# Kernel tuning notes

Hardware: AMD Instinct MI355X
Metric: run time of the kernel (lower is better)

## Reference

```python
import jax, jax.numpy as jnp
import numpy as np

EMBED_DIM = 2048
NUM_HEADS = 32
NUM_SEQS = 8
SEQ_LEN = 1024
TOTAL_TOKENS = NUM_SEQS * SEQ_LEN


def setup_inputs() -> dict:
    key = jax.random.key(0)
    ks = jax.random.split(key, 9)
    E = EMBED_DIM
    std = 0.02
    return {
        "hidden_states": jax.random.normal(ks[0], (TOTAL_TOKENS, E), dtype=jnp.float32),
        "Wq": jax.random.normal(ks[1], (E, E), dtype=jnp.float32) * std,
        "bq": jax.random.normal(ks[2], (E,), dtype=jnp.float32) * std,
        "Wk": jax.random.normal(ks[3], (E, E), dtype=jnp.float32) * std,
        "bk": jax.random.normal(ks[4], (E,), dtype=jnp.float32) * std,
        "Wv": jax.random.normal(ks[5], (E, E), dtype=jnp.float32) * std,
        "bv": jax.random.normal(ks[6], (E,), dtype=jnp.float32) * std,
        "Wo": jax.random.normal(ks[7], (E, E), dtype=jnp.float32) * std,
        "bo": jax.random.normal(ks[8], (E,), dtype=jnp.float32) * std,
        "seq_len": SEQ_LEN,
    }


def reference(hidden_states, Wq, bq, Wk, bk, Wv, bv, Wo, bo, seq_len):
    # OPTAttention (has_cache=False): block-diagonal causal attention over
    # packed ragged sequences; here all NUM_SEQS sequences have length seq_len,
    # so the block-diagonal mask is exactly per-sequence causal attention.
    T, E = hidden_states.shape
    H = NUM_HEADS
    D = E // H
    B = T // seq_len
    scaling = D ** -0.5

    # torch nn.Linear: y = x @ W.T + b
    q = hidden_states @ Wq.T + bq
    k = hidden_states @ Wk.T + bk
    v = hidden_states @ Wv.T + bv

    q = q.reshape(B, seq_len, H, D)
    k = k.reshape(B, seq_len, H, D)
    v = v.reshape(B, seq_len, H, D)

    # [B, H, S, S] attention scores (xformers applies scale to q@k.T)
    scores = jnp.einsum("bqhd,bkhd->bhqk", q, k) * scaling
    causal = jnp.tril(jnp.ones((seq_len, seq_len), dtype=bool))
    scores = jnp.where(causal[None, None, :, :], scores, jnp.finfo(scores.dtype).min)
    probs = jax.nn.softmax(scores, axis=-1)

    attn = jnp.einsum("bhqk,bkhd->bqhd", probs, v)  # [B, S, H, D]
    attn = attn.reshape(T, E)
    return attn @ Wo.T + bo
```

## Files before the change

### kernel.cpp

```cpp
#include <hip/hip_runtime.h>
#include <hip/hip_bf16.h>

typedef __bf16 bf16_t;
typedef __bf16 bf16x8 __attribute__((ext_vector_type(8)));
typedef __bf16 bf16x4 __attribute__((ext_vector_type(4)));
typedef float f32x4 __attribute__((ext_vector_type(4)));
typedef float f32x16 __attribute__((ext_vector_type(16)));
typedef unsigned short u16x8 __attribute__((ext_vector_type(8)));
typedef unsigned int u32x4 __attribute__((ext_vector_type(4)));

#define T_TOK 8192
#define E_DIM 2048
#define NHEAD 32
#define SEQLEN 1024
#define NSEQ 8
#define LDQ 6144

#if __has_builtin(__builtin_amdgcn_exp2f)
#define EXP2F(x) __builtin_amdgcn_exp2f(x)
#else
#define EXP2F(x) exp2f(x)
#endif

static __device__ inline unsigned cvtpk_bf16(float lo, float hi) {
    unsigned r;
    asm("v_cvt_pk_bf16_f32 %0, %1, %2" : "=v"(r) : "v"(lo), "v"(hi));
    return r;
}

static __device__ inline void plswap(unsigned &x, unsigned &y, bool lo_half) {
#if __has_builtin(__builtin_amdgcn_permlane32_swap)
    auto r = __builtin_amdgcn_permlane32_swap(x, y, false, false);
    x = r[0]; y = r[1];
#else
    unsigned xs = __shfl_xor(x, 32), ys = __shfl_xor(y, 32);
    unsigned nx = lo_half ? x : ys;
    unsigned ny = lo_half ? xs : y;
    x = nx; y = ny;
#endif
}

__global__ void cvt_all(const float* __restrict__ hid, const float* __restrict__ Wq,
                        const float* __restrict__ Wk, const float* __restrict__ Wv,
                        const float* __restrict__ Wo, bf16_t* __restrict__ hidB,
                        bf16_t* __restrict__ Wcat, bf16_t* __restrict__ WoB) {
    const int TE4 = (T_TOK * E_DIM) / 4;
    const int EE4 = (E_DIM * E_DIM) / 4;
    const float* src;
    bf16_t* dst;
    int n4, base, nb;
    const int bid = blockIdx.x;
    if (bid < 2048)      { src = hid; dst = hidB;              n4 = TE4; base = 0;    nb = 2048; }
    else if (bid < 2560) { src = Wq;  dst = Wcat;              n4 = EE4; base = 2048; nb = 512; }
    else if (bid < 3072) { src = Wk;  dst = Wcat + 4 * EE4;    n4 = EE4; base = 2560; nb = 512; }
    else if (bid < 3584) { src = Wv;  dst = Wcat + 8 * EE4;    n4 = EE4; base = 3072; nb = 512; }
    else                 { src = Wo;  dst = WoB;               n4 = EE4; base = 3584; nb = 512; }
    const int stride = nb * 256;
    for (int i = (bid - base) * 256 + threadIdx.x; i < n4; i += stride) {
        const float4 v = reinterpret_cast<const float4*>(src)[i];
        bf16x4 o;
        o[0] = (bf16_t)v.x; o[1] = (bf16_t)v.y; o[2] = (bf16_t)v.z; o[3] = (bf16_t)v.w;
        reinterpret_cast<bf16x4*>(dst)[i] = o;
    }
}

template<bool OUT_BF16>
__global__ __launch_bounds__(512, 2)
void gemm256f(const bf16_t* __restrict__ A, const bf16_t* __restrict__ B,
              const float* __restrict__ b0, const float* __restrict__ b1,
              const float* __restrict__ b2, void* __restrict__ Cout,
              int M, int N, float qs, int qlim) {
    constexpr int K = 2048;
    constexpr int NK = K / 32;
    __shared__ alignas(16) unsigned char lds[131072];
    const int tid = threadIdx.x;
    const int wid = tid >> 6, l = tid & 63;
    const int cpx = gridDim.x >> 3;
    const int wg = (blockIdx.x & 7) * cpx + (blockIdx.x >> 3);
    const int nbm = M >> 8;
    const int bm = wg % nbm, bn = wg / nbm;
    const int wrow = (wid >> 2) * 128, wcol = (wid & 3) * 64;
    const int lr = l & 15, lg = l >> 4;

    f32x4 acc[8][4] = {};

    const bf16_t* aBase = A + (size_t)(bm * 256) * K;
    const bf16_t* bBase = B + (size_t)(bn * 256) * K;
    const int sr = l >> 2;
    const int sc = (l & 3) * 16;

    auto stage = [&](int t) {
        unsigned char* base = lds + (t & 3) * 32768;
#pragma unroll
        for (int c = 0; c < 2; ++c) {
            const int chunk = wid * 2 + c;
            const int r = chunk * 16 + sr;
            const int cb = sc ^ (((r >> 1) & 3) << 4);
            __builtin_amdgcn_global_load_lds(
                (const __attribute__((address_space(1))) void*)(aBase + (size_t)r * K + t * 32 + (cb >> 1)),
                (__attribute__((address_space(3))) void*)(base + chunk * 1024), 16, 0, 0);
            __builtin_amdgcn_global_load_lds(
                (const __attribute__((address_space(1))) void*)(bBase + (size_t)r * K + t * 32 + (cb >> 1)),
                (__attribute__((address_space(3))) void*)(base + 16384 + chunk * 1024), 16, 0, 0);
        }
    };

    bf16x8 fa0[8], fb0[4], fa1[8], fb1[4];

    stage(0); stage(1); stage(2);
    asm volatile("s_waitcnt vmcnt(4)" ::: "memory");
    __builtin_amdgcn_s_barrier();
    {
        const unsigned char* Ab = lds;
        const unsigned char* Bb = Ab + 16384;
#pragma unroll
        for (int n = 0; n < 4; ++n) {
            const int r = wcol + n * 16 + lr;
            fb0[n] = *reinterpret_cast<const bf16x8*>(Bb + r * 64 + ((lg * 16) ^ (((r >> 1) & 3) << 4)));
        }
#pragma unroll
        for (int m = 0; m < 8; ++m) {
            const int r = wrow + m * 16 + lr;
            fa0[m] = *reinterpret_cast<const bf16x8*>(Ab + r * 64 + ((lg * 16) ^ (((r >> 1) & 3) << 4)));
        }
    }

    auto step = [&](int t, bf16x8 (&ca)[8], bf16x8 (&cb)[4],
                    bf16x8 (&na)[8], bf16x8 (&nb)[4]) {
        if (t + 3 < NK) stage(t + 3);
        const unsigned char* Nb = lds + ((t + 1) & 3) * 32768;
        const unsigned char* NbB = Nb + 16384;
        __builtin_amdgcn_s_setprio(1);
#pragma unroll
        for (int m = 0; m < 8; ++m) {
            if (m < 4) {
                const int rb = wcol + m * 16 + lr;
                nb[m] = *reinterpret_cast<const bf16x8*>(NbB + rb * 64 + ((lg * 16) ^ (((rb >> 1) & 3) << 4)));
            }
            const int ra = wrow + m * 16 + lr;
            na[m] = *reinterpret_cast<const bf16x8*>(Nb + ra * 64 + ((lg * 16) ^ (((ra >> 1) & 3) << 4)));
#pragma unroll
            for (int n = 0; n < 4; ++n)
                acc[m][n] = __builtin_amdgcn_mfma_f32_16x16x32_bf16(ca[m], cb[n], acc[m][n], 0, 0, 0);
        }
        __builtin_amdgcn_s_setprio(0);
        if (t < NK - 1) {
            if (t + 3 < NK) asm volatile("s_waitcnt vmcnt(4)" ::: "memory");
            else            asm volatile("s_waitcnt vmcnt(0)" ::: "memory");
            __builtin_amdgcn_s_barrier();
        }
    };

#pragma unroll 1
    for (int t = 0; t < NK; t += 2) {
        step(t,     fa0, fb0, fa1, fb1);
        step(t + 1, fa1, fb1, fa0, fb0);
    }

    const int r0 = bm * 256 + wrow + lg * 4;
    const int c0 = bn * 256 + wcol + lr;
#pragma unroll
    for (int n = 0; n < 4; ++n) {
        const int cc = c0 + n * 16;
        const float bias = (cc < 2048) ? b0[cc] : (cc < 4096 ? b1[cc - 2048] : b2[cc - 4096]);
        const float sc2 = (cc < qlim) ? qs : 1.0f;
#pragma unroll
        for (int m = 0; m < 8; ++m)
#pragma unroll
            for (int j = 0; j < 4; ++j) {
                const int rr = r0 + m * 16 + j;
                const float v = (acc[m][n][j] + bias) * sc2;
                if (OUT_BF16) ((bf16_t*)Cout)[(size_t)rr * N + cc] = (bf16_t)v;
                else          ((float*)Cout)[(size_t)rr * N + cc] = v;
            }
    }
}

__global__ __launch_bounds__(512, 2)
void attn_fwd3(const bf16_t* __restrict__ QKV, bf16_t* __restrict__ Og) {
    const int orig = blockIdx.x;
    const int id = (orig & 7) * 64 + (orig >> 3);
    const int grp = id >> 1;
    const int pairIdx = id & 1;
    const int h = grp & 31;
    const int sq = grp >> 5;

    const int tid = threadIdx.x;
    const int w = tid >> 6;
    const int l = tid & 63;
    const int ll = l & 31;
    const int hi = l >> 5;
    const bool lo_half = (hi == 0);

    __shared__ alignas(16) unsigned char lds[65536];

    const bf16_t* Qg = QKV;
    const bf16_t* Kg = QKV + 2048;
    const bf16_t* Vg = QKV + 4096;
    const size_t kvbase = (size_t)(sq * SEQLEN) * LDQ + h * 64;

    bf16x8 vr0, vr1;
    const int vk0 = l * 2;
    const int vd0 = w * 8;

    auto stageK = [&](int kt, int buf) {
#pragma unroll
        for (int c = 0; c < 2; ++c) {
            const int o = (w * 2 + c) * 1024 + l * 16;
            const int r = o >> 7;
            const int swb = (o & 127) ^ ((r & 7) << 4);
            const bf16_t* src = Kg + kvbase + (size_t)(kt * 128 + r) * LDQ + (swb >> 1);
            __builtin_amdgcn_global_load_lds(
                (const __attribute__((address_space(1))) void*)src,
                (__attribute__((address_space(3))) void*)(lds + buf * 16384 + (w * 2 + c) * 1024),
                16, 0, 0);
        }
    };
    auto loadV = [&](int kt) {
        const bf16_t* vp = Vg + kvbase + (size_t)(kt * 128 + vk0) * LDQ + vd0;
        vr0 = *reinterpret_cast<const bf16x8*>(vp);
        vr1 = *reinterpret_cast<const bf16x8*>(vp + LDQ);
    };
    auto writeV = [&](int buf) {
        u16x8 s0 = __builtin_bit_cast(u16x8, vr0);
        u16x8 s1 = __builtin_bit_cast(u16x8, vr1);
        unsigned char* vb = lds + 32768 + buf * 16384;
#pragma unroll
        for (int e = 0; e < 8; ++e) {
            const int d = vd0 + e;
            unsigned off = (unsigned)(d * 256 + vk0 * 2);
            off ^= ((unsigned)((d ^ (d >> 4)) & 15)) << 4;
            *reinterpret_cast<unsigned*>(vb + off) = (unsigned)s0[e] | ((unsigned)s1[e] << 16);
        }
    };

    const unsigned ksw = (unsigned)((l & 7) << 4);
    const unsigned kbase = (unsigned)(ll * 128 + hi * 16);

#pragma unroll 1
    for (int seg = 0; seg < 2; ++seg) {
        const int qt = pairIdx ? (seg ? 2 : 1) : (seg ? 3 : 0);

        const int q_glob = qt * 256 + w * 32 + ll;
        const bf16_t* qp = Qg + (size_t)(sq * SEQLEN + q_glob) * LDQ + h * 64 + hi * 8;
        bf16x8 qf[4];
#pragma unroll
        for (int dc = 0; dc < 4; ++dc)
            qf[dc] = *reinterpret_cast<const bf16x8*>(qp + dc * 16);

        const int nkt = 2 * qt + 2;
        const int q_wave_max = qt * 256 + w * 32 + 31;

        f32x16 oac[2] = {};
        float mrun = -3.0e38f, lsum = 0.f;

        stageK(0, 0);
        loadV(0);
        writeV(0);
        __syncthreads();

        int cur = 0;
        for (int kt = 0; kt < nkt; ++kt) {
            const bool notlast = (kt + 1 < nkt);
            if (notlast) { stageK(kt + 1, cur ^ 1); loadV(kt + 1); }

            if (kt * 128 <= q_wave_max) {
                const unsigned char* Kcur = lds + cur * 16384;
                const unsigned char* Vcur = lds + 32768 + cur * 16384;

                f32x16 st[4];
#pragma unroll
                for (int kh = 0; kh < 4; ++kh) {
                    f32x16 acc = {};
#pragma unroll
                    for (int dc = 0; dc < 4; ++dc) {
                        const unsigned off = (kbase + (unsigned)(kh * 4096 + dc * 32)) ^ ksw;
                        const bf16x8 ka = *reinterpret_cast<const bf16x8*>(Kcur + off);
                        acc = __builtin_amdgcn_mfma_f32_32x32x16_bf16(ka, qf[dc], acc, 0, 0, 0);
                    }
                    st[kh] = acc;
                }

                if (kt >= 2 * qt) {
#pragma unroll
                    for (int kh = 0; kh < 4; ++kh)
#pragma unroll
                        for (int r = 0; r < 16; ++r) {
                            const int kg = kt * 128 + kh * 32 + (r & 3) + 8 * (r >> 2) + 4 * hi;
                            if (kg > q_glob) st[kh][r] = -3.0e38f;
                        }
                }

                float tm = -3.0e38f;
#pragma unroll
                for (int kh = 0; kh < 4; ++kh)
#pragma unroll
                    for (int r = 0; r < 16; ++r) tm = fmaxf(tm, st[kh][r]);
                tm = fmaxf(tm, __shfl_xor(tm, 32));

                if (!__all(tm <= mrun + 8.0f)) {
                    const float mnew = fmaxf(mrun, tm);
                    const float rsc = EXP2F(mrun - mnew);
                    mrun = mnew;
                    lsum *= rsc;
#pragma unroll
                    for (int dh = 0; dh < 2; ++dh)
#pragma unroll
                        for (int r = 0; r < 16; ++r) oac[dh][r] *= rsc;
                }

                float ps = 0.f;
#pragma unroll
                for (int kh = 0; kh < 4; ++kh)
#pragma unroll
                    for (int r = 0; r < 16; ++r) {
                        const float p = EXP2F(st[kh][r] - mrun);
                        st[kh][r] = p;
                        ps += p;
                    }
                ps += __shfl_xor(ps, 32);
                lsum += ps;

                bf16x8 pf[8];
#pragma unroll
                for (int kh = 0; kh < 4; ++kh)
#pragma unroll
                    for (int hc = 0; hc < 2; ++hc) {
                        const int b0i = hc * 8;
                        unsigned a  = cvtpk_bf16(st[kh][b0i + 0], st[kh][b0i + 1]);
                        unsigned b  = cvtpk_bf16(st[kh][b0i + 4], st[kh][b0i + 5]);
                        unsigned a2 = cvtpk_bf16(st[kh][b0i + 2], st[kh][b0i + 3]);
                        unsigned b2 = cvtpk_bf16(st[kh][b0i + 6], st[kh][b0i + 7]);
                        plswap(a, b, lo_half);
                        plswap(a2, b2, lo_half);
                        u32x4 words = { a, a2, b, b2 };
                        pf[kh * 2 + hc] = __builtin_bit_cast(bf16x8, words);
                    }

#pragma unroll
                for (int dh = 0; dh < 2; ++dh) {
                    const int d = dh * 32 + ll;
                    const unsigned vsw = ((unsigned)((d ^ (d >> 4)) & 15)) << 4;
                    const unsigned vbb = (unsigned)(d * 256 + hi * 16);
#pragma unroll
                    for (int kc = 0; kc < 8; ++kc) {
                        const unsigned off = (vbb + (unsigned)(kc * 32)) ^ vsw;
                        const bf16x8 vfr = *reinterpret_cast<const bf16x8*>(Vcur + off);
                        oac[dh] = __builtin_amdgcn_mfma_f32_32x32x16_bf16(vfr, pf[kc], oac[dh], 0, 0, 0);
                    }
                }
            }

            if (notlast) writeV(cur ^ 1);
            __syncthreads();
            cur ^= 1;
        }

        const float inv = 1.0f / lsum;
        bf16_t* op = Og + (size_t)(sq * SEQLEN + q_glob) * E_DIM + h * 64;
#pragma unroll
        for (int dh = 0; dh < 2; ++dh)
#pragma unroll
            for (int rq = 0; rq < 4; ++rq) {
                const int d0 = dh * 32 + 8 * rq + 4 * hi;
                bf16x4 ov;
#pragma unroll
                for (int j = 0; j < 4; ++j)
                    ov[j] = (bf16_t)(oac[dh][rq * 4 + j] * inv);
                *reinterpret_cast<bf16x4*>(op + d0) = ov;
            }
    }
}

extern "C" void kernel_launch(void* const* d_in, const int* in_sizes, int n_in,
                              void* d_out, int out_size, void* d_ws, size_t ws_size,
                              hipStream_t stream) {
    const float* hid = (const float*)d_in[0];
    const float* Wq  = (const float*)d_in[1];
    const float* bq  = (const float*)d_in[2];
    const float* Wk  = (const float*)d_in[3];
    const float* bk  = (const float*)d_in[4];
    const float* Wv  = (const float*)d_in[5];
    const float* bv  = (const float*)d_in[6];
    const float* Wo  = (const float*)d_in[7];
    const float* bo  = (const float*)d_in[8];
    float* out = (float*)d_out;

    const size_t TE = (size_t)T_TOK * E_DIM;
    const size_t EE = (size_t)E_DIM * E_DIM;

    bf16_t* ws   = (bf16_t*)d_ws;
    bf16_t* hidB = ws;
    bf16_t* qkvB = ws + TE;
    bf16_t* Wcat = qkvB + 3 * TE;
    bf16_t* WoB  = Wcat + 3 * EE;

    cvt_all<<<4096, 256, 0, stream>>>(hid, Wq, Wk, Wv, Wo, hidB, Wcat, WoB);

    const float QSCALE = 0.125f * 1.4426950408889634f;

    gemm256f<true><<<dim3((T_TOK / 256) * (LDQ / 256)), 512, 0, stream>>>(
        hidB, Wcat, bq, bk, bv, qkvB, T_TOK, LDQ, QSCALE, 2048);

    attn_fwd3<<<dim3(512), 512, 0, stream>>>(qkvB, hidB);

    gemm256f<false><<<dim3((T_TOK / 256) * (E_DIM / 256)), 512, 0, stream>>>(
        hidB, WoB, bo, bo, bo, out, T_TOK, E_DIM, 1.0f, 0);
}
```

Measured before the change: 397.9 us.

## Restructure GEMM into 8-phase pipeline with K=64 tiles and half-tile staging

Replaces the GEMM main loop with a schedule that uses 64-wide K tiles double-buffered in LDS. Each K step is split into four MFMA quadrants, and staging of the next tiles' A/B halves is interleaved between barrier-separated phases. The aim is to overlap global-to-LDS loads, LDS reads and MFMA more evenly and to halve the number of loop iterations. In exchange it adds many more barriers per iteration, which may stall waves, and it changes the LDS swizzle, which affects bank-conflict behaviour.

```diff
diff --git a/kernel.cpp b/kernel.cpp
--- a/kernel.cpp
+++ b/kernel.cpp
@@ -66,12 +66,12 @@
 
 template<bool OUT_BF16>
 __global__ __launch_bounds__(512, 2)
-void gemm256f(const bf16_t* __restrict__ A, const bf16_t* __restrict__ B,
-              const float* __restrict__ b0, const float* __restrict__ b1,
-              const float* __restrict__ b2, void* __restrict__ Cout,
-              int M, int N, float qs, int qlim) {
+void gemm8p(const bf16_t* __restrict__ A, const bf16_t* __restrict__ B,
+            const float* __restrict__ b0, const float* __restrict__ b1,
+            const float* __restrict__ b2, void* __restrict__ Cout,
+            int M, int N, float qs, int qlim) {
     constexpr int K = 2048;
-    constexpr int NK = K / 32;
+    constexpr int NK = K / 64;
     __shared__ alignas(16) unsigned char lds[131072];
     const int tid = threadIdx.x;
     const int wid = tid >> 6, l = tid & 63;
@@ -84,78 +84,92 @@
 
     f32x4 acc[8][4] = {};
 
-    const bf16_t* aBase = A + (size_t)(bm * 256) * K;
-    const bf16_t* bBase = B + (size_t)(bn * 256) * K;
-    const int sr = l >> 2;
-    const int sc = (l & 3) * 16;
-
-    auto stage = [&](int t) {
-        unsigned char* base = lds + (t & 3) * 32768;
+    const bf16_t* aB = A + (size_t)(bm * 256) * K;
+    const bf16_t* bB = B + (size_t)(bn * 256) * K;
+
+    int rl[2], cbs[2];
+#pragma unroll
+    for (int c = 0; c < 2; ++c) {
+        const int o = (wid * 2 + c) * 1024 + l * 16;
+        rl[c] = o >> 7;
+        cbs[c] = (o & 127) ^ ((rl[c] & 7) << 4);
+    }
+    auto stageHalf = [&](int t, int op, int h) {
+        const bf16_t* s0 = op ? bB : aB;
+        unsigned char* dst = lds + (t & 1) * 65536 + (op * 2 + h) * 16384;
 #pragma unroll
         for (int c = 0; c < 2; ++c) {
-            const int chunk = wid * 2 + c;
-            const int r = chunk * 16 + sr;
-            const int cb = sc ^ (((r >> 1) & 3) << 4);
+            const bf16_t* src = s0 + (size_t)(h * 128 + rl[c]) * K + t * 64 + (cbs[c] >> 1);
             __builtin_amdgcn_global_load_lds(
-                (const __attribute__((address_space(1))) void*)(aBase + (size_t)r * K + t * 32 + (cb >> 1)),
-                (__attribute__((address_space(3))) void*)(base + chunk * 1024), 16, 0, 0);
-            __builtin_amdgcn_global_load_lds(
-                (const __attribute__((address_space(1))) void*)(bBase + (size_t)r * K + t * 32 + (cb >> 1)),
-                (__attribute__((address_space(3))) void*)(base + 16384 + chunk * 1024), 16, 0, 0);
+                (const __attribute__((address_space(1))) void*)src,
+                (__attribute__((address_space(3))) void*)(dst + (wid * 2 + c) * 1024), 16, 0, 0);
         }
     };
 
-    bf16x8 fa0[8], fb0[4], fa1[8], fb1[4];
-
-    stage(0); stage(1); stage(2);
+    const unsigned aSlot = (unsigned)((wrow >> 7) * 16384);
+    const unsigned bSlot = (unsigned)((2 + (wcol >> 7)) * 16384);
+    const unsigned swz = (unsigned)((lr & 7) << 4);
+    const int bRow0 = (wcol & 64);
+
+    bf16x8 af[4][2], bf[4][2];
+    auto loadA = [&](int t, int mh) {
+        const unsigned char* base = lds + (t & 1) * 65536 + aSlot;
+#pragma unroll
+        for (int mi = 0; mi < 4; ++mi)
+#pragma unroll
+            for (int ks = 0; ks < 2; ++ks)
+                af[mi][ks] = *reinterpret_cast<const bf16x8*>(
+                    base + ((mh * 4 + mi) * 16 + lr) * 128 + (((unsigned)(ks * 64 + lg * 16)) ^ swz));
+    };
+    auto loadB2 = [&](int t, int nh) {
+        const unsigned char* base = lds + (t & 1) * 65536 + bSlot;
+#pragma unroll
+        for (int ni = 0; ni < 2; ++ni)
+#pragma unroll
+            for (int ks = 0; ks < 2; ++ks)
+                bf[nh * 2 + ni][ks] = *reinterpret_cast<const bf16x8*>(
+                    base + (bRow0 + (nh * 2 + ni) * 16 + lr) * 128 + (((unsigned)(ks * 64 + lg * 16)) ^ swz));
+    };
+    auto mfmaQuad = [&](int mh, int nh) {
+        __builtin_amdgcn_s_setprio(1);
+#pragma unroll
+        for (int mi = 0; mi < 4; ++mi)
+#pragma unroll
+            for (int ni = 0; ni < 2; ++ni)
+#pragma unroll
+                for (int ks = 0; ks < 2; ++ks)
+                    acc[mh * 4 + mi][nh * 2 + ni] = __builtin_amdgcn_mfma_f32_16x16x32_bf16(
+                        af[mi][ks], bf[nh * 2 + ni][ks], acc[mh * 4 + mi][nh * 2 + ni], 0, 0, 0);
+        __builtin_amdgcn_s_setprio(0);
+    };
+#define LGKM0 do { asm volatile("s_waitcnt lgkmcnt(0)" ::: "memory"); __builtin_amdgcn_sched_barrier(0); } while (0)
+#define BAR __builtin_amdgcn_s_barrier()
+
+    stageHalf(0, 0, 0); stageHalf(0, 1, 0); stageHalf(0, 0, 1); stageHalf(0, 1, 1);
+    stageHalf(1, 0, 0); stageHalf(1, 1, 0);
     asm volatile("s_waitcnt vmcnt(4)" ::: "memory");
-    __builtin_amdgcn_s_barrier();
-    {
-        const unsigned char* Ab = lds;
-        const unsigned char* Bb = Ab + 16384;
-#pragma unroll
-        for (int n = 0; n < 4; ++n) {
-            const int r = wcol + n * 16 + lr;
-            fb0[n] = *reinterpret_cast<const bf16x8*>(Bb + r * 64 + ((lg * 16) ^ (((r >> 1) & 3) << 4)));
-        }
-#pragma unroll
-        for (int m = 0; m < 8; ++m) {
-            const int r = wrow + m * 16 + lr;
-            fa0[m] = *reinterpret_cast<const bf16x8*>(Ab + r * 64 + ((lg * 16) ^ (((r >> 1) & 3) << 4)));
-        }
+    BAR;
+
+#pragma unroll 1
+    for (int t = 0; t < NK; ++t) {
+        loadA(t, 0); loadB2(t, 0);
+        if (t + 1 < NK) stageHalf(t + 1, 0, 1);
+        BAR; LGKM0; mfmaQuad(0, 0); BAR;
+        loadB2(t, 1);
+        if (t + 1 < NK) stageHalf(t + 1, 1, 1);
+        BAR; LGKM0; mfmaQuad(0, 1); BAR;
+        loadA(t, 1);
+        if (t + 2 < NK) stageHalf(t + 2, 0, 0);
+        BAR; LGKM0; mfmaQuad(1, 0); BAR;
+        if (t + 2 < NK) stageHalf(t + 2, 1, 0);
+        BAR; LGKM0; mfmaQuad(1, 1);
+        if (t == NK - 1) break;
+        if (t + 2 < NK) asm volatile("s_waitcnt vmcnt(4)" ::: "memory");
+        else            asm volatile("s_waitcnt vmcnt(0)" ::: "memory");
+        BAR;
     }
-
-    auto step = [&](int t, bf16x8 (&ca)[8], bf16x8 (&cb)[4],
-                    bf16x8 (&na)[8], bf16x8 (&nb)[4]) {
-        if (t + 3 < NK) stage(t + 3);
-        const unsigned char* Nb = lds + ((t + 1) & 3) * 32768;
-        const unsigned char* NbB = Nb + 16384;
-        __builtin_amdgcn_s_setprio(1);
-#pragma unroll
-        for (int m = 0; m < 8; ++m) {
-            if (m < 4) {
-                const int rb = wcol + m * 16 + lr;
-                nb[m] = *reinterpret_cast<const bf16x8*>(NbB + rb * 64 + ((lg * 16) ^ (((rb >> 1) & 3) << 4)));
-            }
-            const int ra = wrow + m * 16 + lr;
-            na[m] = *reinterpret_cast<const bf16x8*>(Nb + ra * 64 + ((lg * 16) ^ (((ra >> 1) & 3) << 4)));
-#pragma unroll
-            for (int n = 0; n < 4; ++n)
-                acc[m][n] = __builtin_amdgcn_mfma_f32_16x16x32_bf16(ca[m], cb[n], acc[m][n], 0, 0, 0);
-        }
-        __builtin_amdgcn_s_setprio(0);
-        if (t < NK - 1) {
-            if (t + 3 < NK) asm volatile("s_waitcnt vmcnt(4)" ::: "memory");
-            else            asm volatile("s_waitcnt vmcnt(0)" ::: "memory");
-            __builtin_amdgcn_s_barrier();
-        }
-    };
-
-#pragma unroll 1
-    for (int t = 0; t < NK; t += 2) {
-        step(t,     fa0, fb0, fa1, fb1);
-        step(t + 1, fa1, fb1, fa0, fb0);
-    }
+#undef LGKM0
+#undef BAR
 
     const int r0 = bm * 256 + wrow + lg * 4;
     const int c0 = bn * 256 + wcol + lr;
@@ -399,11 +413,11 @@
 
     const float QSCALE = 0.125f * 1.4426950408889634f;
 
-    gemm256f<true><<<dim3((T_TOK / 256) * (LDQ / 256)), 512, 0, stream>>>(
+    gemm8p<true><<<dim3((T_TOK / 256) * (LDQ / 256)), 512, 0, stream>>>(
         hidB, Wcat, bq, bk, bv, qkvB, T_TOK, LDQ, QSCALE, 2048);
 
     attn_fwd3<<<dim3(512), 512, 0, stream>>>(qkvB, hidB);
 
-    gemm256f<false><<<dim3((T_TOK / 256) * (E_DIM / 256)), 512, 0, stream>>>(
+    gemm8p<false><<<dim3((T_TOK / 256) * (E_DIM / 256)), 512, 0, stream>>>(
         hidB, WoB, bo, bo, bo, out, T_TOK, E_DIM, 1.0f, 0);
 }
```

Result: no change. 394.6 us (-0.8%).
